# Kernel tuning notes

Hardware: AMD Instinct MI355X
Metric: run time of the kernel (lower is better)

## Reference

```python
import jax, jax.numpy as jnp
import numpy as np

B, C_IN, C_INTER, H, W_DIM = 8, 512, 256, 64, 64


def setup_inputs() -> dict:
    key = jax.random.key(0)
    k1, k2, k3, k4 = jax.random.split(key, 4)
    x = jax.random.normal(k1, (B, C_IN, H, W_DIM), dtype=jnp.float32)
    pem_feats = jax.random.normal(k2, (B, C_INTER, H * W_DIM), dtype=jnp.float32)
    # 1x1 conv weight stored as [out, in] (kernel spatial dims are 1x1)
    W = jax.random.normal(k3, (C_INTER, C_IN), dtype=jnp.float32) * (1.0 / np.sqrt(C_IN))
    bias = jax.random.normal(k4, (C_INTER,), dtype=jnp.float32) * 0.01
    return {"x": x, "pem_feats": pem_feats, "W": W, "bias": bias}


def reference(x, pem_feats, W, bias):
    b, c, h, w = x.shape
    # 1x1 conv == channel-mixing GEMM: [b, inter, h, w]
    proj = jnp.einsum('bchw,oc->bohw', x, W) + bias[None, :, None, None]
    proj = proj.reshape(b, -1, h * w)                      # [b, inter, hw]
    # weights[b,i,j] = <proj[:, i], pem[:, j]>  -> [b, hw, hw], softmax over j
    scores = jnp.einsum('bci,bcj->bij', proj, pem_feats)
    weights = jax.nn.softmax(scores, axis=-1)
    # out[b,k,i] = sum_j weights[b,j,i] * pem[b,k,j]
    eam = jnp.einsum('bji,bkj->bki', weights, pem_feats)   # [b, inter, hw]
    return eam.reshape(b, -1, h, w)
```

## Files before the change

### kernel.cpp

```cpp
#include <hip/hip_runtime.h>
#include <math.h>

#define BATCH 8
#define CIN 512
#define CO 256
#define HW 4096
#define KT 32
#define NSEG 4
#define SEGC 32

typedef unsigned short ushort_t;
typedef unsigned int uint_t;
typedef _Float16 v8h __attribute__((ext_vector_type(8)));
typedef _Float16 v4h __attribute__((ext_vector_type(4)));
typedef float v4f __attribute__((ext_vector_type(4)));
typedef float v16f __attribute__((ext_vector_type(16)));
typedef ushort_t u16x8 __attribute__((ext_vector_type(8)));

__device__ __forceinline__ ushort_t f2h(float f) {
  return __builtin_bit_cast(ushort_t, (_Float16)f);
}
__device__ __forceinline__ v4f mfma16h(v8h a, v8h b, v4f c) {
  return __builtin_amdgcn_mfma_f32_16x16x32_f16(a, b, c, 0, 0, 0);
}
__device__ __forceinline__ v16f mfma32h(v8h a, v8h b, v16f c) {
  return __builtin_amdgcn_mfma_f32_32x32x16_f16(a, b, c, 0, 0, 0);
}
__device__ __forceinline__ v8h lds_frag_h512(const unsigned char* base, int row, int cb) {
  uint4 v = *(const uint4*)(base + row * 512 + (((cb) ^ (row & 7)) << 4));
  return __builtin_bit_cast(v8h, v);
}
__device__ __forceinline__ v8h lds_frag_h128(const unsigned char* base, int row, int cb) {
  uint4 v = *(const uint4*)(base + row * 128 + (((cb) ^ (row & 7)) << 4));
  return __builtin_bit_cast(v8h, v);
}
__device__ __forceinline__ void gll16(const void* g, void* l) {
  __builtin_amdgcn_global_load_lds(
      (const __attribute__((address_space(1))) unsigned int*)g,
      (__attribute__((address_space(3))) unsigned int*)l, 16, 0, 0);
}
#define VMEM_BAR() do {                                            \
    asm volatile("s_waitcnt vmcnt(0) lgkmcnt(0)" ::: "memory");    \
    __builtin_amdgcn_sched_barrier(0);                             \
    __builtin_amdgcn_s_barrier();                                  \
    __builtin_amdgcn_sched_barrier(0);                             \
  } while (0)
#define LDS_BAR() do {                                             \
    asm volatile("s_waitcnt lgkmcnt(0)" ::: "memory");             \
    __builtin_amdgcn_sched_barrier(0);                             \
    __builtin_amdgcn_s_barrier();                                  \
    __builtin_amdgcn_sched_barrier(0);                             \
  } while (0)

__global__ __launch_bounds__(256) void k_w(
    const float* __restrict__ W, ushort_t* __restrict__ w_h) {
  int idx = blockIdx.x * 256 + threadIdx.x;
  size_t off = (size_t)idx * 8;
  float4 v0 = *(const float4*)&W[off];
  float4 v1 = *(const float4*)&W[off + 4];
  float f[8] = {v0.x, v0.y, v0.z, v0.w, v1.x, v1.y, v1.z, v1.w};
  u16x8 h;
#pragma unroll
  for (int j = 0; j < 8; ++j) h[j] = f2h(f[j]);
  *(u16x8*)&w_h[off] = h;
}

__global__ __launch_bounds__(256, 2) void k_proj_mfma(
    const float* __restrict__ x, const ushort_t* __restrict__ w_h,
    const float* __restrict__ bias, ushort_t* __restrict__ proj_h) {
  __shared__ __align__(16) unsigned char L[2][128 * 128];
  __shared__ __align__(16) float Sx[64 * 132];
  const int bid = blockIdx.x;
  const int b = bid & 7;
  const int rest = bid >> 3;
  const int xt = rest & 31;
  const int oh = rest >> 5;
  const int x0 = xt * 128;
  const int t = threadIdx.x;
  const int lane = t & 63, wave = t >> 6;

  v4f acc[2][8];
#pragma unroll
  for (int xf = 0; xf < 2; ++xf)
#pragma unroll
    for (int of = 0; of < 8; ++of) acc[xf][of] = (v4f){0.f, 0.f, 0.f, 0.f};

  float bias_of[8];
#pragma unroll
  for (int of = 0; of < 8; ++of)
    bias_of[of] = bias[oh * 128 + of * 16 + (lane & 15)];

  for (int ch = 0; ch < 8; ++ch) {
    const int c0 = ch * 64;
#pragma unroll
    for (int i = 0; i < 4; ++i) {
      int G = i * 256 + t;
      int r = G >> 3, sl = G & 7;
      int cg = (sl ^ (r & 7)) << 3;
      size_t wsrc = ((size_t)(oh * 128 + r)) * CIN + c0 + cg;
      gll16(&w_h[wsrc], &L[1][(unsigned)((i * 256 + wave * 64) << 4)]);
    }
    {
      int c = t >> 2, xq = t & 3;
      const float* src = &x[((size_t)b * CIN + c0 + c) * HW + x0 + xq * 32];
      float* dst = &Sx[c * 132 + xq * 32];
#pragma unroll
      for (int j = 0; j < 8; ++j)
        *(float4*)&dst[j * 4] = *(const float4*)&src[j * 4];
    }
    __syncthreads();
#pragma unroll
    for (int j = 0; j < 4; ++j) {
      int task = j * 256 + t;
      int xr = task >> 3, gs = task & 7;
      v8h h;
#pragma unroll
      for (int cc = 0; cc < 8; ++cc)
        h[cc] = (_Float16)Sx[(gs * 8 + cc) * 132 + xr];
      *(uint4*)&L[0][xr * 128 + ((gs ^ (xr & 7)) << 4)] =
          __builtin_bit_cast(uint4, h);
    }
    __syncthreads();
#pragma unroll
    for (int st = 0; st < 2; ++st) {
      int cb = st * 4 + (lane >> 4);
      v8h ah0 = lds_frag_h128(L[0], wave * 32 + (lane & 15), cb);
      v8h ah1 = lds_frag_h128(L[0], wave * 32 + 16 + (lane & 15), cb);
#pragma unroll
      for (int of = 0; of < 8; ++of) {
        v8h bh = lds_frag_h128(L[1], of * 16 + (lane & 15), cb);
        acc[0][of] = mfma16h(ah0, bh, acc[0][of]);
        acc[1][of] = mfma16h(ah1, bh, acc[1][of]);
      }
    }
    __syncthreads();
  }

  ushort_t* Th = (ushort_t*)&L[0][0];
#pragma unroll
  for (int xf = 0; xf < 2; ++xf)
#pragma unroll
    for (int of = 0; of < 8; ++of)
#pragma unroll
      for (int r = 0; r < 4; ++r) {
        int x_loc = wave * 32 + xf * 16 + (lane >> 4) * 4 + r;
        int o_loc = of * 16 + (lane & 15);
        Th[x_loc * 128 + o_loc] = f2h(acc[xf][of][r] + bias_of[of]);
      }
  __syncthreads();
  {
    int row = t >> 1, half = t & 1;
    size_t off = ((size_t)b * HW + x0 + row) * CO + oh * 128 + half * 64;
#pragma unroll
    for (int j = 0; j < 8; ++j)
      *(uint4*)&proj_h[off + j * 8] =
          *(const uint4*)&Th[row * 128 + half * 64 + j * 8];
  }
}

__global__ __launch_bounds__(256) void k_tr_pem(
    const float* __restrict__ pem,
    ushort_t* __restrict__ pem_t_h, ushort_t* __restrict__ pem_h) {
  __shared__ float T[64][65];
  const int y0 = blockIdx.x * 64;
  const int c0 = blockIdx.y * 64;
  const int b  = blockIdx.z;
  const int t  = threadIdx.x;
  const int cl = t >> 4;
  const int y4 = (t & 15) * 4;
#pragma unroll
  for (int r = 0; r < 4; ++r) {
    int c = c0 + r * 16 + cl;
    size_t off = ((size_t)b * CO + c) * HW + y0 + y4;
    float4 v = *(const float4*)&pem[off];
    ushort4 h;
    h.x = f2h(v.x); h.y = f2h(v.y); h.z = f2h(v.z); h.w = f2h(v.w);
    *(ushort4*)&pem_h[off] = h;
    T[r * 16 + cl][y4 + 0] = v.x;
    T[r * 16 + cl][y4 + 1] = v.y;
    T[r * 16 + cl][y4 + 2] = v.z;
    T[r * 16 + cl][y4 + 3] = v.w;
  }
  __syncthreads();
  {
    int yl = t >> 2;
    int cs = (t & 3) * 16;
    u16x8 h0, h1;
#pragma unroll
    for (int j = 0; j < 8; ++j) h0[j] = f2h(T[cs + j][yl]);
#pragma unroll
    for (int j = 0; j < 8; ++j) h1[j] = f2h(T[cs + 8 + j][yl]);
    size_t ro = ((size_t)b * HW + y0 + yl) * CO + c0 + cs;
    *(u16x8*)&pem_t_h[ro]     = h0;
    *(u16x8*)&pem_t_h[ro + 8] = h1;
  }
}

__global__ __launch_bounds__(512, 2) void k_stats_f16(
    const ushort_t* __restrict__ proj_h, const ushort_t* __restrict__ pem_t_h,
    float* __restrict__ m_seg, float* __restrict__ d_seg) {
  __shared__ __align__(16) unsigned char pbuf[2][32 * 512];
  const int id = blockIdx.x;
  const int b = id & 7;
  const int rest = id >> 3;
  const int xt = rest & 7;
  const int seg = rest >> 3;
  const int x0 = xt * 512;
  const int t = threadIdx.x;
  const int lane = t & 63, wave = t >> 6;
  const int xw = x0 + wave * 64;

  v8h Ah[4][8];
#pragma unroll
  for (int xf = 0; xf < 4; ++xf) {
    const size_t ro =
        ((size_t)b * HW + xw + xf * 16 + (lane & 15)) * CO + (lane >> 4) * 8;
#pragma unroll
    for (int st = 0; st < 8; ++st)
      Ah[xf][st] = __builtin_bit_cast(v8h, *(const uint4*)&proj_h[ro + st * 32]);
  }

  float m[4][4], d[4][4];
#pragma unroll
  for (int xf = 0; xf < 4; ++xf)
#pragma unroll
    for (int r = 0; r < 4; ++r) { m[xf][r] = -3.0e38f; d[xf][r] = 0.f; }

  auto stage = [&](int bufi, int tt) {
    const int yy0 = tt * 32;
#pragma unroll
    for (int i = 0; i < 2; ++i) {
      int G = i * 512 + t;
      int r = G >> 5, sl = G & 31;
      size_t so = ((size_t)b * HW + yy0 + r) * CO + ((sl ^ (r & 7)) << 3);
      unsigned lb = (unsigned)((i * 512 + wave * 64) << 4);
      gll16(&pem_t_h[so], &pbuf[bufi][lb]);
    }
  };

  const int tt0 = seg * SEGC;
  stage(0, tt0);
  __syncthreads();

  for (int tc = 0; tc < SEGC; ++tc) {
    if (tc + 1 < SEGC) stage((tc + 1) & 1, tt0 + tc + 1);

    const unsigned char* bp = pbuf[tc & 1];
    v4f acc[4][2];
#pragma unroll
    for (int xf = 0; xf < 4; ++xf)
#pragma unroll
      for (int yc = 0; yc < 2; ++yc) acc[xf][yc] = (v4f){0.f, 0.f, 0.f, 0.f};

#pragma unroll
    for (int st = 0; st < 8; ++st) {
#pragma unroll
      for (int yc = 0; yc < 2; ++yc) {
        v8h bh = lds_frag_h512(bp, yc * 16 + (lane & 15), st * 4 + (lane >> 4));
        acc[0][yc] = mfma16h(Ah[0][st], bh, acc[0][yc]);
        acc[1][yc] = mfma16h(Ah[1][st], bh, acc[1][yc]);
        acc[2][yc] = mfma16h(Ah[2][st], bh, acc[2][yc]);
        acc[3][yc] = mfma16h(Ah[3][st], bh, acc[3][yc]);
      }
    }

#pragma unroll
    for (int xf = 0; xf < 4; ++xf) {
      float mx8 = fmaxf(fmaxf(fmaxf(acc[xf][0][0], acc[xf][0][1]),
                              fmaxf(acc[xf][0][2], acc[xf][0][3])),
                        fmaxf(fmaxf(acc[xf][1][0], acc[xf][1][1]),
                              fmaxf(acc[xf][1][2], acc[xf][1][3])));
      float minm = fminf(fminf(m[xf][0], m[xf][1]), fminf(m[xf][2], m[xf][3]));
      if (__any(mx8 > minm + 8.0f)) {
#pragma unroll
        for (int r = 0; r < 4; ++r) {
          float rm = fmaxf(acc[xf][0][r], acc[xf][1][r]);
          rm = fmaxf(rm, __shfl_xor(rm, 1));
          rm = fmaxf(rm, __shfl_xor(rm, 2));
          rm = fmaxf(rm, __shfl_xor(rm, 4));
          rm = fmaxf(rm, __shfl_xor(rm, 8));
          float mn = fmaxf(m[xf][r], rm);
          d[xf][r] *= __expf(m[xf][r] - mn);
          m[xf][r] = mn;
        }
      }
#pragma unroll
      for (int r = 0; r < 4; ++r)
        d[xf][r] += __expf(acc[xf][0][r] - m[xf][r]) +
                    __expf(acc[xf][1][r] - m[xf][r]);
    }
    __syncthreads();
  }

#pragma unroll
  for (int xf = 0; xf < 4; ++xf) {
    float dv[4];
#pragma unroll
    for (int r = 0; r < 4; ++r) {
      float v = d[xf][r];
      v += __shfl_xor(v, 1);
      v += __shfl_xor(v, 2);
      v += __shfl_xor(v, 4);
      v += __shfl_xor(v, 8);
      dv[r] = v;
    }
    if ((lane & 15) == 0) {
      size_t o = ((size_t)(b * NSEG + seg)) * HW + xw + xf * 16 + (lane >> 4) * 4;
      *(float4*)&m_seg[o] = make_float4(m[xf][0], m[xf][1], m[xf][2], m[xf][3]);
      *(float4*)&d_seg[o] = make_float4(dv[0], dv[1], dv[2], dv[3]);
    }
  }
}

__global__ __launch_bounds__(256) void k_red2(
    const float* __restrict__ m_seg, const float* __restrict__ d_seg,
    float* __restrict__ Cx) {
  int idx = blockIdx.x * 256 + threadIdx.x;
  int b = idx >> 12;
  int xx = idx & 4095;
  float ms[NSEG], ds[NSEG];
  float mm = -3.0e38f;
#pragma unroll
  for (int s = 0; s < NSEG; ++s) {
    ms[s] = m_seg[((size_t)(b * NSEG + s)) * HW + xx];
    ds[s] = d_seg[((size_t)(b * NSEG + s)) * HW + xx];
    mm = fmaxf(mm, ms[s]);
  }
  float dd = 0.f;
#pragma unroll
  for (int s = 0; s < NSEG; ++s) dd += ds[s] * __expf(ms[s] - mm);
  Cx[(size_t)b * HW + xx] = mm + __logf(dd);
}

__global__ __launch_bounds__(512, 2) void k_fused(
    const ushort_t* __restrict__ proj_h, const ushort_t* __restrict__ pem_t_h,
    const ushort_t* __restrict__ pem_h, const float* __restrict__ Cx,
    float* __restrict__ out) {
  __shared__ __align__(16) unsigned char Lp[2][64 * 512];
  __shared__ __align__(16) unsigned char Lk[2][256 * 128];
  __shared__ __align__(16) unsigned char Le[128 * 128];
  const int id = blockIdx.x;
  const int b = id & 7;
  const int yt = id >> 3;
  const int y0 = yt * 128;
  const int t = threadIdx.x;
  const int lane = t & 63, wave = t >> 6;
  const int l31 = lane & 31, lh = lane >> 5;
  const int wx = wave & 1, wy = wave >> 1;
  const int kq = wave & 3, yq = wave >> 2;

  v8h Bres[16];
  {
    const size_t ro =
        ((size_t)b * HW + y0 + wy * 32 + l31) * CO + lh * 8;
#pragma unroll
    for (int st = 0; st < 16; ++st)
      Bres[st] = __builtin_bit_cast(v8h, *(const uint4*)&pem_t_h[ro + st * 16]);
  }

  v16f pv[2][2];
#pragma unroll
  for (int kt = 0; kt < 2; ++kt)
#pragma unroll
    for (int yy = 0; yy < 2; ++yy)
#pragma unroll
      for (int r = 0; r < 16; ++r) pv[kt][yy][r] = 0.f;

  auto stage = [&](int bufi, int xt) {
    const int x0s = xt * 64;
#pragma unroll
    for (int i = 0; i < 4; ++i) {
      int G = i * 512 + t;
      int r = G >> 5, sl = G & 31;
      size_t so = ((size_t)b * HW + x0s + r) * CO + ((sl ^ (r & 7)) << 3);
      gll16(&proj_h[so], &Lp[bufi][(unsigned)((i * 512 + wave * 64) << 4)]);
    }
#pragma unroll
    for (int i = 0; i < 4; ++i) {
      int G = i * 512 + t;
      int r = G >> 3, sl = G & 7;
      size_t so = ((size_t)b * CO + r) * HW + x0s + ((sl ^ (r & 7)) << 3);
      gll16(&pem_h[so], &Lk[bufi][(unsigned)((i * 512 + wave * 64) << 4)]);
    }
  };

  stage(0, 0);

  for (int xt = 0; xt < 64; ++xt) {
    const int cur = xt & 1;
    const int x0 = xt * 64;
    VMEM_BAR();

    float4 c4[4];
#pragma unroll
    for (int q = 0; q < 4; ++q)
      c4[q] = *(const float4*)&Cx[(size_t)b * HW + x0 + wx * 32 + 8 * q + 4 * lh];

    if (xt + 1 < 64) stage(cur ^ 1, xt + 1);

    v16f s;
#pragma unroll
    for (int r = 0; r < 16; ++r) s[r] = 0.f;
    __builtin_amdgcn_s_setprio(1);
#pragma unroll
    for (int st = 0; st < 16; ++st) {
      v8h a = lds_frag_h512(Lp[cur], wx * 32 + l31, st * 2 + lh);
      s = mfma32h(a, Bres[st], s);
    }
    __builtin_amdgcn_s_setprio(0);

    {
      int erow = wy * 32 + l31;
#pragma unroll
      for (int q = 0; q < 4; ++q) {
        float cc[4] = {c4[q].x, c4[q].y, c4[q].z, c4[q].w};
        v4h p;
#pragma unroll
        for (int r = 0; r < 4; ++r)
          p[r] = (_Float16)__expf(s[4 * q + r] - cc[r]);
        int gx = wx * 4 + q;
        *(uint2*)(Le + erow * 128 + ((gx ^ (erow & 7)) << 4) + lh * 8) =
            __builtin_bit_cast(uint2, p);
      }
    }
    LDS_BAR();

    __builtin_amdgcn_s_setprio(1);
#pragma unroll
    for (int st = 0; st < 4; ++st) {
      int cb = st * 2 + lh;
      v8h e0 = lds_frag_h128(Le, yq * 64 + l31, cb);
      v8h e1 = lds_frag_h128(Le, yq * 64 + 32 + l31, cb);
      v8h a0 = lds_frag_h128(Lk[cur], kq * 64 + l31, cb);
      v8h a1 = lds_frag_h128(Lk[cur], kq * 64 + 32 + l31, cb);
      pv[0][0] = mfma32h(a0, e0, pv[0][0]);
      pv[0][1] = mfma32h(a0, e1, pv[0][1]);
      pv[1][0] = mfma32h(a1, e0, pv[1][0]);
      pv[1][1] = mfma32h(a1, e1, pv[1][1]);
    }
    __builtin_amdgcn_s_setprio(0);
  }

#pragma unroll
  for (int kt = 0; kt < 2; ++kt)
#pragma unroll
    for (int yy = 0; yy < 2; ++yy)
#pragma unroll
      for (int r = 0; r < 16; ++r) {
        int k = kq * 64 + kt * 32 + (r & 3) + 8 * (r >> 2) + 4 * lh;
        int y = y0 + yq * 64 + yy * 32 + l31;
        out[((size_t)b * CO + k) * HW + y] = pv[kt][yy][r];
      }
}

__global__ __launch_bounds__(256) void k_proj(
    const float* __restrict__ x, const float* __restrict__ W,
    const float* __restrict__ bias, float* __restrict__ proj) {
  __shared__ float As[KT][68];
  __shared__ float Bs[KT][68];
  const int i0 = blockIdx.x * 64;
  const int o0 = blockIdx.y * 64;
  const int b  = blockIdx.z;
  const int t  = threadIdx.x;
  const int tx = t & 15, ty = t >> 4;
  const float* xb = x + (size_t)b * CIN * HW;
  float acc[4][4] = {};
  for (int c0 = 0; c0 < CIN; c0 += KT) {
#pragma unroll
    for (int l = 0; l < 8; ++l) {
      int idx = t + l * 256;
      int o = idx >> 5;
      int c = idx & 31;
      As[c][o] = W[(size_t)(o0 + o) * CIN + c0 + c];
    }
#pragma unroll
    for (int l = 0; l < 2; ++l) {
      int idx4 = t + l * 256;
      int c = idx4 >> 4;
      int i4 = idx4 & 15;
      *(float4*)&Bs[c][i4 * 4] =
          *(const float4*)&xb[(size_t)(c0 + c) * HW + i0 + i4 * 4];
    }
    __syncthreads();
#pragma unroll
    for (int c = 0; c < KT; ++c) {
      float4 a  = *(const float4*)&As[c][tx * 4];
      float4 bv = *(const float4*)&Bs[c][ty * 4];
      float av[4] = {a.x, a.y, a.z, a.w};
      float bb[4] = {bv.x, bv.y, bv.z, bv.w};
#pragma unroll
      for (int u = 0; u < 4; ++u)
#pragma unroll
        for (int v = 0; v < 4; ++v) acc[u][v] += av[u] * bb[v];
    }
    __syncthreads();
  }
  float* pbout = proj + (size_t)b * CO * HW;
#pragma unroll
  for (int u = 0; u < 4; ++u) {
    int o = o0 + tx * 4 + u;
    float bsv = bias[o];
    float4 r;
    r.x = acc[u][0] + bsv; r.y = acc[u][1] + bsv;
    r.z = acc[u][2] + bsv; r.w = acc[u][3] + bsv;
    *(float4*)&pbout[(size_t)o * HW + i0 + ty * 4] = r;
  }
}

__global__ __launch_bounds__(256) void k_stats(
    const float* __restrict__ proj, const float* __restrict__ pem,
    float* __restrict__ Mx, float* __restrict__ Dinv) {
  __shared__ float As[KT][68];
  __shared__ float Bs[KT][68];
  __shared__ float MsS[64][17];
  __shared__ float DsS[64][17];
  const int x0 = blockIdx.x * 64;
  const int b  = blockIdx.y;
  const int t  = threadIdx.x;
  const int tx = t & 15, ty = t >> 4;
  const float* pj = proj + (size_t)b * CO * HW;
  const float* pe = pem + (size_t)b * CO * HW;
  float m[4], d[4];
#pragma unroll
  for (int u = 0; u < 4; ++u) { m[u] = -3.0e38f; d[u] = 0.f; }
  for (int y0 = 0; y0 < HW; y0 += 64) {
    float s[4][4] = {};
    for (int c0 = 0; c0 < CO; c0 += KT) {
#pragma unroll
      for (int l = 0; l < 2; ++l) {
        int idx4 = t + l * 256;
        int c = idx4 >> 4, w4 = idx4 & 15;
        *(float4*)&As[c][w4 * 4] =
            *(const float4*)&pj[(size_t)(c0 + c) * HW + x0 + w4 * 4];
        *(float4*)&Bs[c][w4 * 4] =
            *(const float4*)&pe[(size_t)(c0 + c) * HW + y0 + w4 * 4];
      }
      __syncthreads();
#pragma unroll
      for (int c = 0; c < KT; ++c) {
        float4 a  = *(const float4*)&As[c][tx * 4];
        float4 bv = *(const float4*)&Bs[c][ty * 4];
        float av[4] = {a.x, a.y, a.z, a.w};
        float bb[4] = {bv.x, bv.y, bv.z, bv.w};
#pragma unroll
        for (int u = 0; u < 4; ++u)
#pragma unroll
          for (int v = 0; v < 4; ++v) s[u][v] += av[u] * bb[v];
      }
      __syncthreads();
    }
#pragma unroll
    for (int u = 0; u < 4; ++u) {
      float mv = fmaxf(fmaxf(s[u][0], s[u][1]), fmaxf(s[u][2], s[u][3]));
      if (mv > m[u]) { d[u] *= __expf(m[u] - mv); m[u] = mv; }
      d[u] += __expf(s[u][0] - m[u]) + __expf(s[u][1] - m[u]) +
              __expf(s[u][2] - m[u]) + __expf(s[u][3] - m[u]);
    }
  }
#pragma unroll
  for (int u = 0; u < 4; ++u) { MsS[tx * 4 + u][ty] = m[u]; DsS[tx * 4 + u][ty] = d[u]; }
  __syncthreads();
  if (t < 64) {
    float mm = -3.0e38f;
#pragma unroll
    for (int i = 0; i < 16; ++i) mm = fmaxf(mm, MsS[t][i]);
    float dd = 0.f;
#pragma unroll
    for (int i = 0; i < 16; ++i) dd += DsS[t][i] * __expf(MsS[t][i] - mm);
    Mx[(size_t)b * HW + x0 + t]   = mm;
    Dinv[(size_t)b * HW + x0 + t] = 1.0f / dd;
  }
}

__global__ __launch_bounds__(256) void k_out(
    const float* __restrict__ proj, const float* __restrict__ pem,
    const float* __restrict__ Mx, const float* __restrict__ Dinv,
    float* __restrict__ out) {
  __shared__ float As[KT][68];
  __shared__ float Bs[KT][68];
  __shared__ float E[64][68];
  const int y0 = blockIdx.x * 64;
  const int b  = blockIdx.y;
  const int t  = threadIdx.x;
  const int tx = t & 15, ty = t >> 4;
  const int kg = t >> 3, yg = t & 7;
  const float* pj = proj + (size_t)b * CO * HW;
  const float* pe = pem + (size_t)b * CO * HW;
  const float* Mb = Mx + (size_t)b * HW;
  const float* Db = Dinv + (size_t)b * HW;
  float acc[8][8] = {};
  for (int x0 = 0; x0 < HW; x0 += 64) {
    float s[4][4] = {};
    for (int c0 = 0; c0 < CO; c0 += KT) {
#pragma unroll
      for (int l = 0; l < 2; ++l) {
        int idx4 = t + l * 256;
        int c = idx4 >> 4, w4 = idx4 & 15;
        *(float4*)&As[c][w4 * 4] =
            *(const float4*)&pj[(size_t)(c0 + c) * HW + x0 + w4 * 4];
        *(float4*)&Bs[c][w4 * 4] =
            *(const float4*)&pe[(size_t)(c0 + c) * HW + y0 + w4 * 4];
      }
      __syncthreads();
#pragma unroll
      for (int c = 0; c < KT; ++c) {
        float4 a  = *(const float4*)&As[c][tx * 4];
        float4 bv = *(const float4*)&Bs[c][ty * 4];
        float av[4] = {a.x, a.y, a.z, a.w};
        float bb[4] = {bv.x, bv.y, bv.z, bv.w};
#pragma unroll
        for (int u = 0; u < 4; ++u)
#pragma unroll
          for (int v = 0; v < 4; ++v) s[u][v] += av[u] * bb[v];
      }
      __syncthreads();
    }
#pragma unroll
    for (int u = 0; u < 4; ++u) {
      int xr = x0 + tx * 4 + u;
      float mm = Mb[xr];
      float di = Db[xr];
      E[tx * 4 + u][ty * 4 + 0] = __expf(s[u][0] - mm) * di;
      E[tx * 4 + u][ty * 4 + 1] = __expf(s[u][1] - mm) * di;
      E[tx * 4 + u][ty * 4 + 2] = __expf(s[u][2] - mm) * di;
      E[tx * 4 + u][ty * 4 + 3] = __expf(s[u][3] - mm) * di;
    }
    __syncthreads();
    for (int xi = 0; xi < 64; xi += 4) {
      float4 p[8];
#pragma unroll
      for (int u = 0; u < 8; ++u)
        p[u] = *(const float4*)&pe[(size_t)(kg * 8 + u) * HW + x0 + xi];
#pragma unroll
      for (int j = 0; j < 4; ++j) {
        float4 e0 = *(const float4*)&E[xi + j][yg * 8];
        float4 e1 = *(const float4*)&E[xi + j][yg * 8 + 4];
        float evv[8] = {e0.x, e0.y, e0.z, e0.w, e1.x, e1.y, e1.z, e1.w};
#pragma unroll
        for (int u = 0; u < 8; ++u) {
          float a = (j == 0) ? p[u].x : (j == 1) ? p[u].y : (j == 2) ? p[u].z : p[u].w;
#pragma unroll
          for (int v = 0; v < 8; ++v) acc[u][v] += a * evv[v];
        }
      }
    }
    __syncthreads();
  }
#pragma unroll
  for (int u = 0; u < 8; ++u) {
    int k = kg * 8 + u;
    float4 r0, r1;
    r0.x = acc[u][0]; r0.y = acc[u][1]; r0.z = acc[u][2]; r0.w = acc[u][3];
    r1.x = acc[u][4]; r1.y = acc[u][5]; r1.z = acc[u][6]; r1.w = acc[u][7];
    float* ob = out + ((size_t)b * CO + k) * HW + y0 + yg * 8;
    *(float4*)&ob[0] = r0;
    *(float4*)&ob[4] = r1;
  }
}

extern "C" void kernel_launch(void* const* d_in, const int* in_sizes, int n_in,
                              void* d_out, int out_size, void* d_ws, size_t ws_size,
                              hipStream_t stream) {
  const float* x    = (const float*)d_in[0];
  const float* pem  = (const float*)d_in[1];
  const float* W    = (const float*)d_in[2];
  const float* bias = (const float*)d_in[3];
  float* out = (float*)d_out;

  const size_t NS   = (size_t)BATCH * HW * CO;
  const size_t NS2  = (size_t)BATCH * HW * CIN;
  const size_t HWB  = (size_t)BATCH * HW;
  const size_t SEGN = (size_t)BATCH * NSEG * HW;
  const size_t WN   = (size_t)CO * CIN;

  unsigned char* basep = (unsigned char*)d_ws;
  ushort_t* proj_h   = (ushort_t*)basep;
  ushort_t* pem_t_h  = proj_h + NS;
  ushort_t* pem_h    = pem_t_h + NS;
  float*    Cxp      = (float*)(pem_h + NS);
  float*    m_seg    = Cxp + HWB;
  float*    d_seg    = m_seg + SEGN;
  ushort_t* xt_h     = (ushort_t*)(d_seg + SEGN);
  ushort_t* w_h      = xt_h + NS2;

  const size_t need = 3 * NS * 2 + HWB * 4 + 2 * SEGN * 4 + NS2 * 2 + WN * 2;

  if (ws_size < need) {
    float* proj = (float*)d_ws;
    float* Mx2  = proj + NS;
    float* Di2  = Mx2 + HWB;
    const size_t need_f = (NS + 2 * HWB) * sizeof(float);
    if (ws_size < need_f) return;
    k_proj <<<dim3(HW / 64, CO / 64, BATCH), 256, 0, stream>>>(x, W, bias, proj);
    k_stats<<<dim3(HW / 64, BATCH),          256, 0, stream>>>(proj, pem, Mx2, Di2);
    k_out  <<<dim3(HW / 64, BATCH),          256, 0, stream>>>(proj, pem, Mx2, Di2, out);
    return;
  }

  k_w<<<64, 256, 0, stream>>>(W, w_h);
  k_proj_mfma<<<512, 256, 0, stream>>>(x, w_h, bias, proj_h);
  k_tr_pem<<<dim3(HW / 64, CO / 64, BATCH), 256, 0, stream>>>(pem, pem_t_h, pem_h);

  k_stats_f16<<<256, 512, 0, stream>>>(proj_h, pem_t_h, m_seg, d_seg);
  k_red2<<<128, 256, 0, stream>>>(m_seg, d_seg, Cxp);
  k_fused<<<256, 512, 0, stream>>>(proj_h, pem_t_h, pem_h, Cxp, out);
}
```

Before: 318.8 us.

## Keep softmax probabilities in registers, split-K PV across wave pairs, widen LDS swizzle

The fused attention kernel no longer writes exp(scores) to an LDS tile and re-reads it after a barrier. It packs the probabilities into fp16 pairs with cvt_pkrtz, swaps halves between lanes with a cross-lane shuffle to form MFMA B operands in registers, and drops the intra-iteration LDS barrier. Each wave now accumulates all 256 output channels for its 32 columns over half of each x-tile, so two waves split K and their partial sums are reduced through LDS at the end. The LDS swizzle is also widened from row&7 to row&31 for the 512-byte rows. This raises the accumulator register footprint (8 v16f per wave), which may hurt occupancy or cause spills, and adds a final reduction step.

```diff
diff --git a/kernel.cpp b/kernel.cpp
--- a/kernel.cpp
+++ b/kernel.cpp
@@ -20,14 +20,17 @@
 __device__ __forceinline__ ushort_t f2h(float f) {
   return __builtin_bit_cast(ushort_t, (_Float16)f);
 }
+__device__ __forceinline__ uint_t pkrtz(float lo, float hi) {
+  return __builtin_bit_cast(uint_t, __builtin_amdgcn_cvt_pkrtz(lo, hi));
+}
 __device__ __forceinline__ v4f mfma16h(v8h a, v8h b, v4f c) {
   return __builtin_amdgcn_mfma_f32_16x16x32_f16(a, b, c, 0, 0, 0);
 }
 __device__ __forceinline__ v16f mfma32h(v8h a, v8h b, v16f c) {
   return __builtin_amdgcn_mfma_f32_32x32x16_f16(a, b, c, 0, 0, 0);
 }
-__device__ __forceinline__ v8h lds_frag_h512(const unsigned char* base, int row, int cb) {
-  uint4 v = *(const uint4*)(base + row * 512 + (((cb) ^ (row & 7)) << 4));
+__device__ __forceinline__ v8h lds_frag_h512w(const unsigned char* base, int row, int cb) {
+  uint4 v = *(const uint4*)(base + row * 512 + (((cb) ^ (row & 31)) << 4));
   return __builtin_bit_cast(v8h, v);
 }
 __device__ __forceinline__ v8h lds_frag_h128(const unsigned char* base, int row, int cb) {
@@ -232,7 +235,7 @@
     for (int i = 0; i < 2; ++i) {
       int G = i * 512 + t;
       int r = G >> 5, sl = G & 31;
-      size_t so = ((size_t)b * HW + yy0 + r) * CO + ((sl ^ (r & 7)) << 3);
+      size_t so = ((size_t)b * HW + yy0 + r) * CO + ((sl ^ (r & 31)) << 3);
       unsigned lb = (unsigned)((i * 512 + wave * 64) << 4);
       gll16(&pem_t_h[so], &pbuf[bufi][lb]);
     }
@@ -256,7 +259,7 @@
     for (int st = 0; st < 8; ++st) {
 #pragma unroll
       for (int yc = 0; yc < 2; ++yc) {
-        v8h bh = lds_frag_h512(bp, yc * 16 + (lane & 15), st * 4 + (lane >> 4));
+        v8h bh = lds_frag_h512w(bp, yc * 16 + (lane & 15), st * 4 + (lane >> 4));
         acc[0][yc] = mfma16h(Ah[0][st], bh, acc[0][yc]);
         acc[1][yc] = mfma16h(Ah[1][st], bh, acc[1][yc]);
         acc[2][yc] = mfma16h(Ah[2][st], bh, acc[2][yc]);
@@ -336,9 +339,9 @@
     const ushort_t* __restrict__ proj_h, const ushort_t* __restrict__ pem_t_h,
     const ushort_t* __restrict__ pem_h, const float* __restrict__ Cx,
     float* __restrict__ out) {
-  __shared__ __align__(16) unsigned char Lp[2][64 * 512];
-  __shared__ __align__(16) unsigned char Lk[2][256 * 128];
-  __shared__ __align__(16) unsigned char Le[128 * 128];
+  __shared__ __align__(16) unsigned char SMEM[128 * 1024];
+  unsigned char (*Lp)[64 * 512] = (unsigned char (*)[64 * 512])(SMEM);
+  unsigned char (*Lk)[256 * 128] = (unsigned char (*)[256 * 128])(SMEM + 64 * 1024);
   const int id = blockIdx.x;
   const int b = id & 7;
   const int yt = id >> 3;
@@ -346,25 +349,21 @@
   const int t = threadIdx.x;
   const int lane = t & 63, wave = t >> 6;
   const int l31 = lane & 31, lh = lane >> 5;
-  const int wx = wave & 1, wy = wave >> 1;
-  const int kq = wave & 3, yq = wave >> 2;
+  const int half = wave & 1, ys = wave >> 1;
 
   v8h Bres[16];
   {
-    const size_t ro =
-        ((size_t)b * HW + y0 + wy * 32 + l31) * CO + lh * 8;
+    const size_t ro = ((size_t)b * HW + y0 + ys * 32 + l31) * CO + lh * 8;
 #pragma unroll
     for (int st = 0; st < 16; ++st)
       Bres[st] = __builtin_bit_cast(v8h, *(const uint4*)&pem_t_h[ro + st * 16]);
   }
 
-  v16f pv[2][2];
-#pragma unroll
-  for (int kt = 0; kt < 2; ++kt)
-#pragma unroll
-    for (int yy = 0; yy < 2; ++yy)
-#pragma unroll
-      for (int r = 0; r < 16; ++r) pv[kt][yy][r] = 0.f;
+  v16f pv[8];
+#pragma unroll
+  for (int kt = 0; kt < 8; ++kt)
+#pragma unroll
+    for (int r = 0; r < 16; ++r) pv[kt][r] = 0.f;
 
   auto stage = [&](int bufi, int xt) {
     const int x0s = xt * 64;
@@ -372,7 +371,7 @@
     for (int i = 0; i < 4; ++i) {
       int G = i * 512 + t;
       int r = G >> 5, sl = G & 31;
-      size_t so = ((size_t)b * HW + x0s + r) * CO + ((sl ^ (r & 7)) << 3);
+      size_t so = ((size_t)b * HW + x0s + r) * CO + ((sl ^ (r & 31)) << 3);
       gll16(&proj_h[so], &Lp[bufi][(unsigned)((i * 512 + wave * 64) << 4)]);
     }
 #pragma unroll
@@ -391,11 +390,6 @@
     const int x0 = xt * 64;
     VMEM_BAR();
 
-    float4 c4[4];
-#pragma unroll
-    for (int q = 0; q < 4; ++q)
-      c4[q] = *(const float4*)&Cx[(size_t)b * HW + x0 + wx * 32 + 8 * q + 4 * lh];
-
     if (xt + 1 < 64) stage(cur ^ 1, xt + 1);
 
     v16f s;
@@ -404,53 +398,75 @@
     __builtin_amdgcn_s_setprio(1);
 #pragma unroll
     for (int st = 0; st < 16; ++st) {
-      v8h a = lds_frag_h512(Lp[cur], wx * 32 + l31, st * 2 + lh);
+      v8h a = lds_frag_h512w(Lp[cur], half * 32 + l31, st * 2 + lh);
       s = mfma32h(a, Bres[st], s);
     }
     __builtin_amdgcn_s_setprio(0);
 
+    uint_t d[8];
     {
-      int erow = wy * 32 + l31;
+      const float* cxb = &Cx[(size_t)b * HW + x0 + half * 32 + 4 * lh];
 #pragma unroll
       for (int q = 0; q < 4; ++q) {
-        float cc[4] = {c4[q].x, c4[q].y, c4[q].z, c4[q].w};
-        v4h p;
-#pragma unroll
-        for (int r = 0; r < 4; ++r)
-          p[r] = (_Float16)__expf(s[4 * q + r] - cc[r]);
-        int gx = wx * 4 + q;
-        *(uint2*)(Le + erow * 128 + ((gx ^ (erow & 7)) << 4) + lh * 8) =
-            __builtin_bit_cast(uint2, p);
-      }
-    }
-    LDS_BAR();
+        float4 c4 = *(const float4*)&cxb[8 * q];
+        d[2 * q]     = pkrtz(__expf(s[4 * q + 0] - c4.x),
+                             __expf(s[4 * q + 1] - c4.y));
+        d[2 * q + 1] = pkrtz(__expf(s[4 * q + 2] - c4.z),
+                             __expf(s[4 * q + 3] - c4.w));
+      }
+    }
+    uint_t p[8];
+#pragma unroll
+    for (int j = 0; j < 8; ++j)
+      p[j] = (uint_t)__shfl_xor((int)d[j], 32);
+    uint4 w0, w1;
+    if (lh == 0) {
+      w0 = make_uint4(d[0], d[1], p[0], p[1]);
+      w1 = make_uint4(d[4], d[5], p[4], p[5]);
+    } else {
+      w0 = make_uint4(p[2], p[3], d[2], d[3]);
+      w1 = make_uint4(p[6], p[7], d[6], d[7]);
+    }
+    v8h B0 = __builtin_bit_cast(v8h, w0);
+    v8h B1 = __builtin_bit_cast(v8h, w1);
 
     __builtin_amdgcn_s_setprio(1);
 #pragma unroll
-    for (int st = 0; st < 4; ++st) {
-      int cb = st * 2 + lh;
-      v8h e0 = lds_frag_h128(Le, yq * 64 + l31, cb);
-      v8h e1 = lds_frag_h128(Le, yq * 64 + 32 + l31, cb);
-      v8h a0 = lds_frag_h128(Lk[cur], kq * 64 + l31, cb);
-      v8h a1 = lds_frag_h128(Lk[cur], kq * 64 + 32 + l31, cb);
-      pv[0][0] = mfma32h(a0, e0, pv[0][0]);
-      pv[0][1] = mfma32h(a0, e1, pv[0][1]);
-      pv[1][0] = mfma32h(a1, e0, pv[1][0]);
-      pv[1][1] = mfma32h(a1, e1, pv[1][1]);
+    for (int kt = 0; kt < 8; ++kt) {
+      v8h a0 = lds_frag_h128(Lk[cur], kt * 32 + l31, half * 4 + 0 + lh);
+      pv[kt] = mfma32h(a0, B0, pv[kt]);
+      v8h a1 = lds_frag_h128(Lk[cur], kt * 32 + l31, half * 4 + 2 + lh);
+      pv[kt] = mfma32h(a1, B1, pv[kt]);
     }
     __builtin_amdgcn_s_setprio(0);
   }
 
-#pragma unroll
-  for (int kt = 0; kt < 2; ++kt)
-#pragma unroll
-    for (int yy = 0; yy < 2; ++yy)
-#pragma unroll
-      for (int r = 0; r < 16; ++r) {
-        int k = kq * 64 + kt * 32 + (r & 3) + 8 * (r >> 2) + 4 * lh;
-        int y = y0 + yq * 64 + yy * 32 + l31;
-        out[((size_t)b * CO + k) * HW + y] = pv[kt][yy][r];
-      }
+  LDS_BAR();
+  {
+    float* red = (float*)SMEM;
+    if (half == 1) {
+      float* dst = red + (size_t)ys * 8192;
+#pragma unroll
+      for (int kt = 0; kt < 8; ++kt)
+#pragma unroll
+        for (int r = 0; r < 16; ++r)
+          dst[(kt * 16 + r) * 64 + lane] = pv[kt][r];
+    }
+    __syncthreads();
+    if (half == 0) {
+      const float* src = red + (size_t)ys * 8192;
+#pragma unroll
+      for (int kt = 0; kt < 8; ++kt) {
+#pragma unroll
+        for (int r = 0; r < 16; ++r) {
+          float v = pv[kt][r] + src[(kt * 16 + r) * 64 + lane];
+          int k = kt * 32 + (r & 3) + 8 * (r >> 2) + 4 * lh;
+          int y = y0 + ys * 32 + l31;
+          out[((size_t)b * CO + k) * HW + y] = v;
+        }
+      }
+    }
+  }
 }
 
 __global__ __launch_bounds__(256) void k_proj(
```

Result: slower. 353.5 us (+10.9%).
